# Optimization experiments

Measured on AMD Instinct MI355X. Metric: run time of the kernel, lower is better.

Reference implementation:

```python
import jax, jax.numpy as jnp
import numpy as np

B, T, H = 2, 2048, 2048          # batch, seq, hidden
NH, NKV, HD = 16, 8, 128         # heads, kv heads, head_dim
EPS = 1e-6
ROPE_THETA = 1e6
NEG = -1e9


def _rope_tables(t, d, dtype=jnp.float32):
    inv_freq = 1.0 / (ROPE_THETA ** (jnp.arange(0, d, 2, dtype=jnp.float32) / d))
    freqs = jnp.arange(t, dtype=jnp.float32)[:, None] * inv_freq[None, :]  # [t, d/2]
    emb = jnp.concatenate([freqs, freqs], axis=-1)                          # [t, d]
    return jnp.cos(emb).astype(dtype), jnp.sin(emb).astype(dtype)


def _rotate_half(x):
    x1, x2 = jnp.split(x, 2, axis=-1)
    return jnp.concatenate([-x2, x1], axis=-1)


def _rmsnorm(x, w):
    xf = x.astype(jnp.float32)
    var = jnp.mean(xf * xf, axis=-1, keepdims=True)
    return (w * (xf * jax.lax.rsqrt(var + EPS)).astype(x.dtype))


def setup_inputs() -> dict:
    key = jax.random.key(0)
    ks = jax.random.split(key, 6)
    x = jax.random.normal(ks[0], (B, T, H), dtype=jnp.float32)
    # additive causal mask: 0 on/below diagonal, large negative above
    causal = jnp.tril(jnp.ones((T, T), dtype=bool))
    attn_mask = jnp.where(causal, 0.0, NEG).astype(jnp.float32)[None, None]
    s = 1.0 / np.sqrt(H)
    Wq = jax.random.normal(ks[1], (H, NH * HD), dtype=jnp.float32) * s
    Wk = jax.random.normal(ks[2], (H, NKV * HD), dtype=jnp.float32) * s
    Wv = jax.random.normal(ks[3], (H, NKV * HD), dtype=jnp.float32) * s
    Wo = jax.random.normal(ks[4], (NH * HD, H), dtype=jnp.float32) * (1.0 / np.sqrt(NH * HD))
    q_norm_w = jnp.ones((HD,), dtype=jnp.float32)
    k_norm_w = jnp.ones((HD,), dtype=jnp.float32)
    return {"x": x, "attn_mask": attn_mask, "Wq": Wq, "Wk": Wk, "Wv": Wv,
            "Wo": Wo, "q_norm_w": q_norm_w, "k_norm_w": k_norm_w}


def reference(x, attn_mask, Wq, Wk, Wv, Wo, q_norm_w, k_norm_w):
    b, t, _ = x.shape
    n_rep = NH // NKV
    q = (x @ Wq).reshape(b, t, NH, HD).transpose(0, 2, 1, 3)    # [b,nh,t,d]
    k = (x @ Wk).reshape(b, t, NKV, HD).transpose(0, 2, 1, 3)   # [b,nkv,t,d]
    v = (x @ Wv).reshape(b, t, NKV, HD).transpose(0, 2, 1, 3)
    q = _rmsnorm(q, q_norm_w)
    k = _rmsnorm(k, k_norm_w)
    cos, sin = _rope_tables(t, HD, x.dtype)                      # [t,d]
    cos = cos[None, None]; sin = sin[None, None]                 # [1,1,t,d]
    q = q * cos + _rotate_half(q) * sin
    k = k * cos + _rotate_half(k) * sin
    # repeat kv heads for GQA
    k = jnp.repeat(k, n_rep, axis=1)                             # [b,nh,t,d]
    v = jnp.repeat(v, n_rep, axis=1)
    scale = HD ** -0.5
    scores = jnp.einsum('bhqd,bhkd->bhqk', q, k) * scale + attn_mask
    probs = jax.nn.softmax(scores.astype(jnp.float32), axis=-1).astype(q.dtype)
    ctx = jnp.einsum('bhqk,bhkd->bhqd', probs, v)
    ctx = ctx.transpose(0, 2, 1, 3).reshape(b, t, NH * HD)
    return ctx @ Wo
```

## Files before the change

kernel.cpp:

```cpp
#include <hip/hip_runtime.h>
#include <stdint.h>

#define B_   2
#define T_   2048
#define H_   2048
#define NH_  16
#define NKV_ 8
#define HD_  128

typedef unsigned short u16;
typedef __bf16 v8bf __attribute__((ext_vector_type(8)));
typedef short  v8s  __attribute__((ext_vector_type(8)));
typedef float  v4f  __attribute__((ext_vector_type(4)));

static __device__ __forceinline__ float b2f(u16 h) {
  union { unsigned u; float f; } x; x.u = ((unsigned)h) << 16; return x.f;
}
static __device__ __forceinline__ u16 f2b(float f) {
  union { float f; unsigned u; } x; x.f = f;
  unsigned r = x.u + 0x7fffu + ((x.u >> 16) & 1u);
  return (u16)(r >> 16);
}
static __device__ __forceinline__ v8bf asbf(v8s x) { return __builtin_bit_cast(v8bf, x); }

__global__ __launch_bounds__(256) void cvt_f32_bf16(
    const float* __restrict__ src, u16* __restrict__ dst, unsigned n4)
{
  unsigned i = blockIdx.x * 256 + threadIdx.x;
  const unsigned stride = gridDim.x * 256;
  for (; i < n4; i += stride) {
    const float4 v = ((const float4*)src)[i];
    ushort4 o;
    o.x = f2b(v.x); o.y = f2b(v.y); o.z = f2b(v.z); o.w = f2b(v.w);
    ((ushort4*)dst)[i] = o;
  }
}

__global__ __launch_bounds__(256) void transpose_f32_bf16(
    const float* __restrict__ src, u16* __restrict__ dst, int R, int C)
{
  __shared__ u16 tile[64][66];
  const int tc = blockIdx.x * 64, tr = blockIdx.y * 64;
  const int lc = threadIdx.x & 63, lr = threadIdx.x >> 6;
  #pragma unroll
  for (int rr = 0; rr < 64; rr += 4)
    tile[rr + lr][lc] = f2b(src[(size_t)(tr + rr + lr) * C + tc + lc]);
  __syncthreads();
  #pragma unroll
  for (int rr = 0; rr < 64; rr += 4)
    dst[(size_t)(tc + rr + lr) * R + tr + lc] = tile[lc][rr + lr];
}

__global__ __launch_bounds__(256) void transpose_bf16(
    const u16* __restrict__ src, u16* __restrict__ dst, int R, int C,
    long srcZ, long dstZ)
{
  __shared__ u16 tile[64][66];
  const int z = blockIdx.z;
  src += (size_t)z * srcZ;
  dst += (size_t)z * dstZ;
  const int tc = blockIdx.x * 64, tr = blockIdx.y * 64;
  const int lc = threadIdx.x & 63, lr = threadIdx.x >> 6;
  #pragma unroll
  for (int rr = 0; rr < 64; rr += 4)
    tile[rr + lr][lc] = src[(size_t)(tr + rr + lr) * C + tc + lc];
  __syncthreads();
  #pragma unroll
  for (int rr = 0; rr < 64; rr += 4)
    dst[(size_t)(tc + rr + lr) * R + tr + lc] = tile[lc][rr + lr];
}

__global__ __launch_bounds__(256) void fill_vones(u16* __restrict__ VhTp)
{
  const int z = blockIdx.x >> 4, ri = blockIdx.x & 15;
  const u16 val = (ri == 0) ? (u16)0x3F80 : (u16)0;
  u16* row = VhTp + ((size_t)z * 144 + 128 + ri) * T_;
  for (int i = threadIdx.x; i < T_; i += 256) row[i] = val;
}

template <bool F32OUT>
__global__ __launch_bounds__(256) void gemm_bt(
    const u16* __restrict__ A, const u16* __restrict__ Bt, void* __restrict__ Cout,
    int M, int N, int K)
{
  __shared__ __align__(16) u16 As[128 * 32];
  __shared__ __align__(16) u16 Bs[128 * 32];
  const int tid  = threadIdx.x;
  const int wave = tid >> 6, lane = tid & 63;
  const int l15  = lane & 15, quad = lane >> 4;
  const int wm   = (wave >> 1) * 64, wn = (wave & 1) * 64;
  const int m0   = blockIdx.y * 128, n0 = blockIdx.x * 128;

  const int srow = wave * 32 + (lane >> 2);
  const int scol = (lane & 3) * 8;

  v4f acc[4][4];
  const v4f z4 = {0.f, 0.f, 0.f, 0.f};
  #pragma unroll
  for (int i = 0; i < 4; ++i)
    #pragma unroll
    for (int j = 0; j < 4; ++j) acc[i][j] = z4;

  for (int k0 = 0; k0 < K; k0 += 32) {
    __syncthreads();
    #pragma unroll
    for (int l = 0; l < 2; ++l) {
      const u16* ga = A + (size_t)(m0 + srow + l * 16) * K + k0 + scol;
      __builtin_amdgcn_global_load_lds(
          (const __attribute__((address_space(1))) void*)ga,
          (__attribute__((address_space(3))) void*)((char*)As + (wave * 2 + l) * 1024),
          16, 0, 0);
      const u16* gb = Bt + (size_t)(n0 + srow + l * 16) * K + k0 + scol;
      __builtin_amdgcn_global_load_lds(
          (const __attribute__((address_space(1))) void*)gb,
          (__attribute__((address_space(3))) void*)((char*)Bs + (wave * 2 + l) * 1024),
          16, 0, 0);
    }
    __builtin_amdgcn_s_waitcnt(0);
    __syncthreads();
    v8s a[4], b[4];
    #pragma unroll
    for (int mi = 0; mi < 4; ++mi)
      a[mi] = *(const v8s*)&As[(wm + mi * 16 + l15) * 32 + quad * 8];
    #pragma unroll
    for (int ni = 0; ni < 4; ++ni)
      b[ni] = *(const v8s*)&Bs[(wn + ni * 16 + l15) * 32 + quad * 8];
    #pragma unroll
    for (int mi = 0; mi < 4; ++mi)
      #pragma unroll
      for (int ni = 0; ni < 4; ++ni)
        acc[mi][ni] = __builtin_amdgcn_mfma_f32_16x16x32_bf16(
            asbf(a[mi]), asbf(b[ni]), acc[mi][ni], 0, 0, 0);
  }
  #pragma unroll
  for (int mi = 0; mi < 4; ++mi)
    #pragma unroll
    for (int ni = 0; ni < 4; ++ni)
      #pragma unroll
      for (int r = 0; r < 4; ++r) {
        const int m = m0 + wm + mi * 16 + quad * 4 + r;
        const int n = n0 + wn + ni * 16 + l15;
        if (F32OUT) ((float*)Cout)[(size_t)m * N + n] = acc[mi][ni][r];
        else        ((u16*)Cout)[(size_t)m * N + n]  = f2b(acc[mi][ni][r]);
      }
}

__global__ __launch_bounds__(256) void norm_rope_scatter(
    const u16* __restrict__ QKV, const float* __restrict__ qw, const float* __restrict__ kw,
    u16* __restrict__ Qh, u16* __restrict__ Kh, u16* __restrict__ Vh)
{
  const int vid  = blockIdx.x * 4 + (threadIdx.x >> 6);
  const int lane = threadIdx.x & 63;
  const int head = vid & 31;
  const int bt   = vid >> 5;
  const int b    = bt >> 11, t = bt & (T_ - 1);
  const int colbase = head < 16 ? head * 128
                    : (head < 24 ? 2048 + (head - 16) * 128
                                 : 3072 + (head - 24) * 128);
  const u16* src = QKV + (size_t)bt * 4096 + colbase;
  const u16 r1 = src[lane], r2 = src[lane + 64];
  if (head >= 24) {
    u16* dst = Vh + ((size_t)(b * NKV_ + (head - 24)) * T_ + t) * 128;
    dst[lane] = r1; dst[lane + 64] = r2;
    return;
  }
  float x1 = b2f(r1), x2 = b2f(r2);
  float ss = x1 * x1 + x2 * x2;
  #pragma unroll
  for (int d = 1; d < 64; d <<= 1) ss += __shfl_xor(ss, d, 64);
  const float rinv = rsqrtf(ss * (1.f / 128.f) + 1e-6f);
  const float* w = head < 16 ? qw : kw;
  const float n1 = x1 * rinv * w[lane];
  const float n2 = x2 * rinv * w[lane + 64];
  const float invf = exp2f(-(float)lane * (19.931568569324174f / 64.f));
  const float ang  = (float)t * invf;
  const float c = cosf(ang), s = sinf(ang);
  const float o1 = n1 * c - n2 * s;
  const float o2 = n2 * c + n1 * s;
  u16* dst = (head < 16)
      ? Qh + ((size_t)(b * NH_ + head) * T_ + t) * 128
      : Kh + ((size_t)(b * NKV_ + (head - 16)) * T_ + t) * 128;
  dst[lane]      = f2b(o1);
  dst[lane + 64] = f2b(o2);
}

__global__ __launch_bounds__(256) void attn_fused2(
    const u16* __restrict__ Qh, const u16* __restrict__ Kh,
    const u16* __restrict__ VhTp, u16* __restrict__ ctx)
{
  __shared__ __align__(16) u16 Plds[4][32 * 40];
  __shared__ v4f Olds[2][18][64];

  const int wave = threadIdx.x >> 6, lane = threadIdx.x & 63;
  const int l15 = lane & 15, quad = lane >> 4;
  const int bid = blockIdx.x;
  const int g = bid & 31, h = (bid >> 5) & 15, b = bid >> 9;
  const int pairsel = wave >> 1;
  const int half    = wave & 1;
  const int qt = pairsel ? (63 - g) : g;
  const int q0 = qt * 32;
  const int nt = qt + 1;
  const int jt0 = half ? (nt >> 1) : 0;
  const int jt1 = half ? nt : (nt >> 1);

  const u16* Qb = Qh   + (size_t)(b * NH_ + h) * T_ * 128;
  const u16* Kb = Kh   + (size_t)(b * NKV_ + (h >> 1)) * T_ * 128;
  const u16* Vb = VhTp + (size_t)(b * NKV_ + (h >> 1)) * 144 * T_;
  u16* Pl = Plds[wave];

  const float k2 = 0.12751740f;
  const float C2 = 17.0f;
  const v4f z4 = {0.f, 0.f, 0.f, 0.f};

  v8s qf[2][4];
  #pragma unroll
  for (int mi = 0; mi < 2; ++mi)
    #pragma unroll
    for (int c = 0; c < 4; ++c)
      qf[mi][c] = *(const v8s*)(Qb + (size_t)(q0 + mi * 16 + l15) * 128 + c * 32 + quad * 8);

  v4f o[2][9];
  #pragma unroll
  for (int mi = 0; mi < 2; ++mi)
    #pragma unroll
    for (int di = 0; di < 9; ++di) o[mi][di] = z4;

  for (int jt = jt0; jt < jt1; ++jt) {
    const int j0 = jt * 32;
    v4f s[2][2];
    s[0][0] = z4; s[0][1] = z4; s[1][0] = z4; s[1][1] = z4;
    #pragma unroll
    for (int ni = 0; ni < 2; ++ni)
      #pragma unroll
      for (int c = 0; c < 4; ++c) {
        const v8s kf = *(const v8s*)(Kb + (size_t)(j0 + ni * 16 + l15) * 128 + c * 32 + quad * 8);
        s[0][ni] = __builtin_amdgcn_mfma_f32_16x16x32_bf16(asbf(qf[0][c]), asbf(kf), s[0][ni], 0, 0, 0);
        s[1][ni] = __builtin_amdgcn_mfma_f32_16x16x32_bf16(asbf(qf[1][c]), asbf(kf), s[1][ni], 0, 0, 0);
      }
    const bool diag = (j0 == q0);
    #pragma unroll
    for (int mi = 0; mi < 2; ++mi)
      #pragma unroll
      for (int r = 0; r < 4; ++r) {
        const int qrow = mi * 16 + quad * 4 + r;
        float u0 = fmaf(s[mi][0][r], k2, -C2);
        float u1 = fmaf(s[mi][1][r], k2, -C2);
        if (diag) {
          if (l15 > qrow)      u0 = -1e30f;
          if (16 + l15 > qrow) u1 = -1e30f;
        }
        Pl[qrow * 40 + l15]      = f2b(exp2f(u0));
        Pl[qrow * 40 + 16 + l15] = f2b(exp2f(u1));
      }
    v8s pf[2];
    pf[0] = *(const v8s*)&Pl[l15 * 40 + quad * 8];
    pf[1] = *(const v8s*)&Pl[(16 + l15) * 40 + quad * 8];
    #pragma unroll
    for (int di = 0; di < 9; ++di) {
      const v8s vt = *(const v8s*)(Vb + (size_t)(di * 16 + l15) * T_ + j0 + quad * 8);
      o[0][di] = __builtin_amdgcn_mfma_f32_16x16x32_bf16(asbf(pf[0]), asbf(vt), o[0][di], 0, 0, 0);
      o[1][di] = __builtin_amdgcn_mfma_f32_16x16x32_bf16(asbf(pf[1]), asbf(vt), o[1][di], 0, 0, 0);
    }
  }

  if (half == 1) {
    #pragma unroll
    for (int mi = 0; mi < 2; ++mi)
      #pragma unroll
      for (int di = 0; di < 9; ++di)
        Olds[pairsel][mi * 9 + di][lane] = o[mi][di];
  }
  __syncthreads();
  if (half == 1) return;
  #pragma unroll
  for (int mi = 0; mi < 2; ++mi)
    #pragma unroll
    for (int di = 0; di < 9; ++di)
      o[mi][di] += Olds[pairsel][mi * 9 + di][lane];

  #pragma unroll
  for (int mi = 0; mi < 2; ++mi) {
    float inv[4];
    #pragma unroll
    for (int r = 0; r < 4; ++r) {
      const float lb = __shfl(o[mi][8][r], lane & 48, 64);
      inv[r] = 1.f / lb;
    }
    #pragma unroll
    for (int di = 0; di < 8; ++di)
      #pragma unroll
      for (int r = 0; r < 4; ++r) {
        const int t   = q0 + mi * 16 + quad * 4 + r;
        const int col = h * 128 + di * 16 + l15;
        ctx[(size_t)(b * T_ + t) * (NH_ * HD_) + col] = f2b(o[mi][di][r] * inv[r]);
      }
  }
}

extern "C" void kernel_launch(void* const* d_in, const int* in_sizes, int n_in,
                              void* d_out, int out_size, void* d_ws, size_t ws_size,
                              hipStream_t stream) {
  (void)in_sizes; (void)n_in; (void)out_size; (void)ws_size;
  const float* x  = (const float*)d_in[0];
  const float* Wq = (const float*)d_in[2];
  const float* Wk = (const float*)d_in[3];
  const float* Wv = (const float*)d_in[4];
  const float* Wo = (const float*)d_in[5];
  const float* Wo_ = Wo;
  const float* qw = (const float*)d_in[6];
  const float* kw = (const float*)d_in[7];
  float* out = (float*)d_out;

  char* ws = (char*)d_ws;
  u16* WoT   = (u16*)(ws);
  u16* WqkvT = (u16*)(ws + 8388608);
  u16* Vh    = (u16*)(ws + 8388608);
  u16* VhTp  = (u16*)(ws + 16777216);
  u16* x_bf  = (u16*)(ws + 25165824);
  u16* ctx   = (u16*)(ws + 26214400);
  u16* Qh    = (u16*)(ws + 42991616);
  u16* Kh    = (u16*)(ws + 59768832);
  u16* QKV = (u16*)d_out;

  cvt_f32_bf16<<<2048, 256, 0, stream>>>(x, x_bf, 2097152u);
  transpose_f32_bf16<<<dim3(32, 32), 256, 0, stream>>>(Wq, WqkvT,               2048, 2048);
  transpose_f32_bf16<<<dim3(16, 32), 256, 0, stream>>>(Wk, WqkvT + 2048 * 2048, 2048, 1024);
  transpose_f32_bf16<<<dim3(16, 32), 256, 0, stream>>>(Wv, WqkvT + 3072 * 2048, 2048, 1024);
  transpose_f32_bf16<<<dim3(32, 32), 256, 0, stream>>>(Wo_, WoT,                2048, 2048);

  gemm_bt<false><<<dim3(32, 32), 256, 0, stream>>>(x_bf, WqkvT, QKV, 4096, 4096, 2048);

  norm_rope_scatter<<<dim3(32768), 256, 0, stream>>>(QKV, qw, kw, Qh, Kh, Vh);
  fill_vones<<<256, 256, 0, stream>>>(VhTp);
  transpose_bf16<<<dim3(2, 32, 16), 256, 0, stream>>>(Vh, VhTp, 2048, 128,
                                                      (long)2048 * 128, (long)144 * 2048);

  attn_fused2<<<dim3(1024), 256, 0, stream>>>(Qh, Kh, VhTp, ctx);

  gemm_bt<true><<<dim3(16, 32), 256, 0, stream>>>(ctx, WoT, (void*)out, 4096, 2048, 2048);
}
```

Measured before the change: 467.4 us.

## Prefetch K tiles with register double buffering and remap blocks by KV head

```diff
diff --git a/kernel.cpp b/kernel.cpp
--- a/kernel.cpp
+++ b/kernel.cpp
@@ -189,12 +189,17 @@
     const u16* __restrict__ VhTp, u16* __restrict__ ctx)
 {
   __shared__ __align__(16) u16 Plds[4][32 * 40];
-  __shared__ v4f Olds[2][18][64];
+  __shared__ v4f Olds[2][9][64];
 
   const int wave = threadIdx.x >> 6, lane = threadIdx.x & 63;
   const int l15 = lane & 15, quad = lane >> 4;
   const int bid = blockIdx.x;
-  const int g = bid & 31, h = (bid >> 5) & 15, b = bid >> 9;
+  const int kv3 = bid & 7;
+  const int up  = bid >> 3;
+  const int g   = up & 31;
+  const int bh  = up >> 5;
+  const int b   = bh >> 1;
+  const int h   = kv3 * 2 + (bh & 1);
   const int pairsel = wave >> 1;
   const int half    = wave & 1;
   const int qt = pairsel ? (63 - g) : g;
@@ -225,6 +230,17 @@
     #pragma unroll
     for (int di = 0; di < 9; ++di) o[mi][di] = z4;
 
+  v8s kf[2][2][4];
+  {
+    const int j0 = jt0 * 32;
+    #pragma unroll
+    for (int ni = 0; ni < 2; ++ni)
+      #pragma unroll
+      for (int c = 0; c < 4; ++c)
+        kf[0][ni][c] = *(const v8s*)(Kb + (size_t)(j0 + ni * 16 + l15) * 128 + c * 32 + quad * 8);
+  }
+
+  int cur = 0;
   for (int jt = jt0; jt < jt1; ++jt) {
     const int j0 = jt * 32;
     v4f s[2][2];
@@ -233,10 +249,18 @@
     for (int ni = 0; ni < 2; ++ni)
       #pragma unroll
       for (int c = 0; c < 4; ++c) {
-        const v8s kf = *(const v8s*)(Kb + (size_t)(j0 + ni * 16 + l15) * 128 + c * 32 + quad * 8);
-        s[0][ni] = __builtin_amdgcn_mfma_f32_16x16x32_bf16(asbf(qf[0][c]), asbf(kf), s[0][ni], 0, 0, 0);
-        s[1][ni] = __builtin_amdgcn_mfma_f32_16x16x32_bf16(asbf(qf[1][c]), asbf(kf), s[1][ni], 0, 0, 0);
+        s[0][ni] = __builtin_amdgcn_mfma_f32_16x16x32_bf16(asbf(qf[0][c]), asbf(kf[cur][ni][c]), s[0][ni], 0, 0, 0);
+        s[1][ni] = __builtin_amdgcn_mfma_f32_16x16x32_bf16(asbf(qf[1][c]), asbf(kf[cur][ni][c]), s[1][ni], 0, 0, 0);
       }
+    {
+      const int jn = (jt + 1 < jt1) ? jt + 1 : jt;
+      const int jn0 = jn * 32;
+      #pragma unroll
+      for (int ni = 0; ni < 2; ++ni)
+        #pragma unroll
+        for (int c = 0; c < 4; ++c)
+          kf[cur ^ 1][ni][c] = *(const v8s*)(Kb + (size_t)(jn0 + ni * 16 + l15) * 128 + c * 32 + quad * 8);
+    }
     const bool diag = (j0 == q0);
     #pragma unroll
     for (int mi = 0; mi < 2; ++mi)
@@ -261,22 +285,23 @@
       o[0][di] = __builtin_amdgcn_mfma_f32_16x16x32_bf16(asbf(pf[0]), asbf(vt), o[0][di], 0, 0, 0);
       o[1][di] = __builtin_amdgcn_mfma_f32_16x16x32_bf16(asbf(pf[1]), asbf(vt), o[1][di], 0, 0, 0);
     }
-  }
-
-  if (half == 1) {
-    #pragma unroll
-    for (int mi = 0; mi < 2; ++mi)
+    cur ^= 1;
+  }
+
+  #pragma unroll
+  for (int mi = 0; mi < 2; ++mi) {
+    if (half == 1)
       #pragma unroll
       for (int di = 0; di < 9; ++di)
-        Olds[pairsel][mi * 9 + di][lane] = o[mi][di];
-  }
-  __syncthreads();
+        Olds[pairsel][di][lane] = o[mi][di];
+    __syncthreads();
+    if (half == 0)
+      #pragma unroll
+      for (int di = 0; di < 9; ++di)
+        o[mi][di] += Olds[pairsel][di][lane];
+    __syncthreads();
+  }
   if (half == 1) return;
-  #pragma unroll
-  for (int mi = 0; mi < 2; ++mi)
-    #pragma unroll
-    for (int di = 0; di < 9; ++di)
-      o[mi][di] += Olds[pairsel][mi * 9 + di][lane];
 
   #pragma unroll
   for (int mi = 0; mi < 2; ++mi) {
@@ -306,7 +331,6 @@
   const float* Wk = (const float*)d_in[3];
   const float* Wv = (const float*)d_in[4];
   const float* Wo = (const float*)d_in[5];
-  const float* Wo_ = Wo;
   const float* qw = (const float*)d_in[6];
   const float* kw = (const float*)d_in[7];
   float* out = (float*)d_out;
@@ -326,7 +350,7 @@
   transpose_f32_bf16<<<dim3(32, 32), 256, 0, stream>>>(Wq, WqkvT,               2048, 2048);
   transpose_f32_bf16<<<dim3(16, 32), 256, 0, stream>>>(Wk, WqkvT + 2048 * 2048, 2048, 1024);
   transpose_f32_bf16<<<dim3(16, 32), 256, 0, stream>>>(Wv, WqkvT + 3072 * 2048, 2048, 1024);
-  transpose_f32_bf16<<<dim3(32, 32), 256, 0, stream>>>(Wo_, WoT,                2048, 2048);
+  transpose_f32_bf16<<<dim3(32, 32), 256, 0, stream>>>(Wo, WoT,                 2048, 2048);
 
   gemm_bt<false><<<dim3(32, 32), 256, 0, stream>>>(x_bf, WqkvT, QKV, 4096, 4096, 2048);
 
```

After: 667.0 us. +42.7%, slower.
